# Performance work log

Hardware: AMD Instinct MI355X
Metric: run time of the kernel (lower is better)

The kernel has to match this reference:

```python
import jax, jax.numpy as jnp
import numpy as np

NEG_SLOPE = 0.2  # GATConv default leaky_relu slope


def setup_inputs() -> dict:
    key = jax.random.key(0)
    ks = jax.random.split(key, 5)
    B, C, N, H, F, k = 8, 128, 4096, 4, 128, 16
    return {
        "x": jax.random.normal(ks[0], (B, C, N, 1), dtype=jnp.float32),
        "W": jax.random.normal(ks[1], (C, H * F), dtype=jnp.float32) * 0.05,
        "att_src": jax.random.normal(ks[2], (H, F), dtype=jnp.float32) * 0.05,
        "att_dst": jax.random.normal(ks[3], (H, F), dtype=jnp.float32) * 0.05,
        "bias": jax.random.normal(ks[4], (F,), dtype=jnp.float32) * 0.05,
        "k": k,
    }


def reference(x, W, att_src, att_dst, bias, k):
    B, C, N, _ = x.shape
    H, F = att_src.shape
    xf = jnp.transpose(x[..., 0], (0, 2, 1))  # [B, N, C] node features

    # --- per-batch kNN graph in feature space (loop=True: self included) ---
    sq = jnp.sum(xf * xf, axis=-1)  # [B, N]
    # squared Euclidean distances [B, N, N]
    dist = sq[:, :, None] + sq[:, None, :] - 2.0 * jnp.einsum("bnc,bmc->bnm", xf, xf)
    _, nbr = jax.lax.top_k(-dist, k)  # [B, N, k] indices of k nearest (incl. self)

    # --- GATConv (concat=False -> average heads) ---
    h = jnp.einsum("bnc,chf->bnhf", xf, W.reshape(C, H, F))  # [B, N, H, F]
    a_src = jnp.sum(h * att_src, axis=-1)  # [B, N, H]
    a_dst = jnp.sum(h * att_dst, axis=-1)  # [B, N, H]

    gather = jax.vmap(lambda a, idx: a[idx])  # batched fancy-index
    a_src_n = gather(a_src, nbr)  # [B, N, k, H]
    h_n = gather(h, nbr)          # [B, N, k, H, F]

    e = jax.nn.leaky_relu(a_src_n + a_dst[:, :, None, :], NEG_SLOPE)  # [B, N, k, H]
    alpha = jax.nn.softmax(e, axis=2)  # softmax over each node's k incoming edges
    out = jnp.sum(alpha[..., None] * h_n, axis=2)  # [B, N, H, F]
    out = jnp.mean(out, axis=2) + bias  # [B, N, F]
    return jnp.transpose(out, (0, 2, 1))[..., None]  # [B, F, N, 1]
```

## Files before the change

### kernel.cpp

```cpp
#include <hip/hip_runtime.h>
#include <hip/hip_bf16.h>

#define BB 8
#define CC 128
#define NN 4096
#define HH 4
#define FF 128
#define KK 16
#define HF 512
#define CAPH 128
#define LCAP 32

typedef __attribute__((ext_vector_type(8))) short short8v;
typedef __attribute__((ext_vector_type(8))) unsigned short ushort8v;
typedef __attribute__((ext_vector_type(4))) float f32x4;

__device__ __forceinline__ float bf2f(unsigned int u) {
  return __uint_as_float(u << 16);
}

__device__ __forceinline__ unsigned short f2bf(float f) {
  unsigned int u = __float_as_uint(f);
  unsigned int lsb = (u >> 16) & 1u;
  u += 0x7fffu + lsb;
  return (unsigned short)(u >> 16);
}

__device__ __forceinline__ unsigned int umin2(unsigned int a, unsigned int b) {
  return a < b ? a : b;
}
__device__ __forceinline__ unsigned int umin3(unsigned int a, unsigned int b, unsigned int c) {
  return umin2(umin2(a, b), c);
}

__device__ __forceinline__ void gload16(const void* gsrc, void* ldst) {
  __builtin_amdgcn_global_load_lds(
      (const __attribute__((address_space(1))) unsigned int*)gsrc,
      (__attribute__((address_space(3))) unsigned int*)ldst, 16, 0, 0);
}

__launch_bounds__(256)
__global__ void k_split(const float* __restrict__ x,
                        float* __restrict__ xt,
                        unsigned short* __restrict__ xhi,
                        float* __restrict__ hsq) {
  __shared__ float Ls[CC][65];
  int b = blockIdx.x >> 6, nb = blockIdx.x & 63;
  int n0 = nb * 64;
  int tid = threadIdx.x;
  const float* xb = x + (size_t)b * CC * NN;

  for (int i = tid; i < CC * 64; i += 256) {
    int c = i >> 6, nl = i & 63;
    Ls[c][nl] = xb[(size_t)c * NN + n0 + nl];
  }
  __syncthreads();

  int n = tid >> 2, part = tid & 3;
  int node = b * NN + n0 + n;
  float sum = 0.f;
#pragma unroll
  for (int g = 0; g < 4; ++g) {
    float v[8];
    ushort8v ph;
#pragma unroll
    for (int j = 0; j < 8; ++j) {
      int c = part * 32 + g * 8 + j;
      v[j] = Ls[c][n];
      ph[j] = f2bf(v[j]);
      sum += v[j] * v[j];
    }
    float4 f0 = {v[0], v[1], v[2], v[3]};
    float4 f1 = {v[4], v[5], v[6], v[7]};
    *(float4*)&xt[(size_t)node * CC + part * 32 + g * 8] = f0;
    *(float4*)&xt[(size_t)node * CC + part * 32 + g * 8 + 4] = f1;
    *(ushort8v*)&xhi[(size_t)node * CC + part * 32 + g * 8] = ph;
  }
  sum += __shfl_xor(sum, 1, 64);
  sum += __shfl_xor(sum, 2, 64);
  if (part == 0) hsq[node] = 0.5f * sum;
}

__global__ void k_wpack(const float* __restrict__ W,
                        unsigned short* __restrict__ Whi,
                        unsigned short* __restrict__ Wlo) {
  int g = blockIdx.x * 256 + threadIdx.x;
  int kg = g & 3, r16 = (g >> 2) & 15, ks = (g >> 6) & 3, ct = g >> 8;
  int hf = ct * 16 + r16;
  int c0 = ks * 32 + kg * 8;
  ushort8v ph, pl;
#pragma unroll
  for (int j = 0; j < 8; ++j) {
    float v = W[(size_t)(c0 + j) * HF + hf];
    unsigned short hb = f2bf(v);
    ph[j] = hb;
    pl[j] = f2bf(v - bf2f(hb));
  }
  *(ushort8v*)&Whi[(size_t)g * 8] = ph;
  *(ushort8v*)&Wlo[(size_t)g * 8] = pl;
}

__launch_bounds__(256)
__global__ void k_tauscan(const unsigned short* __restrict__ xhi,
                          const float* __restrict__ hsq,
                          unsigned int* __restrict__ keys16) {
  __shared__ short8v AS[2][256];
  __shared__ unsigned int mv[4][16][33];
  int bx = blockIdx.x;
  int b = bx & 7, rest = bx >> 3;
  int qg = rest >> 1, sh = rest & 1;
  int w = threadIdx.x >> 6, lane = threadIdx.x & 63;
  int qcol = lane & 15, kg = lane >> 4;
  int base = b * NN;
  int q = base + qg * 64 + w * 16 + qcol;
  int t0 = sh * 32;

  const short8v* XH = (const short8v*)xhi;
  short8v bh0 = XH[(size_t)q * 16 + kg];
  short8v bh1 = XH[(size_t)q * 16 + 4 + kg];
  short8v bh2 = XH[(size_t)q * 16 + 8 + kg];
  short8v bh3 = XH[(size_t)q * 16 + 12 + kg];

  int snode = w * 4 + (lane >> 4);
  int sgran = (lane & 15) ^ (snode & 15);

  gload16(xhi + ((size_t)(base + t0 * 16 + snode)) * 128 + sgran * 8, &AS[0][w * 64]);
  __syncthreads();

  unsigned int bd[8];
  unsigned int worst = 0;
  int cur = 0;

#pragma unroll 1
  for (int lt = 0; lt < 32; ++lt) {
    if (lt + 1 < 32)
      gload16(xhi + ((size_t)(base + (t0 + lt + 1) * 16 + snode)) * 128 + sgran * 8,
              &AS[cur ^ 1][w * 64]);
    short8v ah0 = AS[cur][qcol * 16 + ((0 + kg) ^ qcol)];
    short8v ah1 = AS[cur][qcol * 16 + ((4 + kg) ^ qcol)];
    short8v ah2 = AS[cur][qcol * 16 + ((8 + kg) ^ qcol)];
    short8v ah3 = AS[cur][qcol * 16 + ((12 + kg) ^ qcol)];
    f32x4 acc = {0.f, 0.f, 0.f, 0.f};
    acc = __builtin_amdgcn_mfma_f32_16x16x32_bf16(ah0, bh0, acc, 0, 0, 0);
    acc = __builtin_amdgcn_mfma_f32_16x16x32_bf16(ah1, bh1, acc, 0, 0, 0);
    acc = __builtin_amdgcn_mfma_f32_16x16x32_bf16(ah2, bh2, acc, 0, 0, 0);
    acc = __builtin_amdgcn_mfma_f32_16x16x32_bf16(ah3, bh3, acc, 0, 0, 0);
    float4 hs = *(const float4*)&hsq[base + (t0 + lt) * 16 + kg * 4];
    float hsa[4] = {hs.x, hs.y, hs.z, hs.w};

    if (lt < 2) {
#pragma unroll
      for (int r = 0; r < 4; ++r) {
        float tv = acc[r] - hsa[r] + 512.0f;
        bd[lt * 4 + r] = (__float_as_uint(tv) & ~1023u) | (1023u - (unsigned)(lt * 4 + r));
      }
      if (lt == 1) {
        unsigned int m0 = umin3(bd[0], bd[1], bd[2]);
        m0 = umin3(m0, bd[3], bd[4]);
        m0 = umin3(m0, bd[5], bd[6]);
        worst = umin2(m0, bd[7]);
      }
    } else {
#pragma unroll
      for (int r = 0; r < 4; ++r) {
        float tv = acc[r] - hsa[r] + 512.0f;
        unsigned int key = (__float_as_uint(tv) & ~1023u) | (1023u - (unsigned)(lt * 4 + r));
        if (key > worst) {
#pragma unroll
          for (int i = 0; i < 8; ++i) bd[i] = (bd[i] == worst) ? key : bd[i];
          unsigned int m0 = umin3(bd[0], bd[1], bd[2]);
          m0 = umin3(m0, bd[3], bd[4]);
          m0 = umin3(m0, bd[5], bd[6]);
          worst = umin2(m0, bd[7]);
        }
      }
    }
    __syncthreads();
    cur ^= 1;
  }

#pragma unroll
  for (int i = 0; i < 8; ++i) mv[w][qcol][kg * 8 + i] = bd[i];
  __syncthreads();

  if (lane < 16) {
    unsigned int tb[16];
#pragma unroll
    for (int i = 0; i < 16; ++i) tb[i] = mv[w][lane][i];
    unsigned int w0 = umin3(tb[0], tb[1], tb[2]);
    w0 = umin3(w0, tb[3], tb[4]);
    w0 = umin3(w0, tb[5], tb[6]);
    w0 = umin2(w0, tb[7]);
    unsigned int w1 = umin3(tb[8], tb[9], tb[10]);
    w1 = umin3(w1, tb[11], tb[12]);
    w1 = umin3(w1, tb[13], tb[14]);
    w1 = umin2(w1, tb[15]);
    unsigned int wst = umin2(w0, w1);
    for (int j = 16; j < 32; ++j) {
      unsigned int v = mv[w][lane][j];
      if (v > wst) {
        bool done = false;
#pragma unroll
        for (int i = 0; i < 16; ++i) {
          bool m = (!done) && (tb[i] == wst);
          done = done || m;
          tb[i] = m ? v : tb[i];
        }
        unsigned int a0 = umin3(tb[0], tb[1], tb[2]);
        a0 = umin3(a0, tb[3], tb[4]);
        a0 = umin3(a0, tb[5], tb[6]);
        a0 = umin2(a0, tb[7]);
        unsigned int a1 = umin3(tb[8], tb[9], tb[10]);
        a1 = umin3(a1, tb[11], tb[12]);
        a1 = umin3(a1, tb[13], tb[14]);
        a1 = umin2(a1, tb[15]);
        wst = umin2(a0, a1);
      }
    }
    int qq = base + qg * 64 + w * 16 + lane;
    unsigned int* o = keys16 + ((size_t)qq * 2 + sh) * 16;
#pragma unroll
    for (int i = 0; i < 16; ++i) o[i] = tb[i];
  }
}

__launch_bounds__(256)
__global__ void k_taumerge(const unsigned int* __restrict__ keys16,
                           float* __restrict__ thr) {
  int q = blockIdx.x * 256 + threadIdx.x;
  const unsigned int* kp = keys16 + (size_t)q * 32;
  unsigned int tb[16];
#pragma unroll
  for (int i = 0; i < 16; ++i) tb[i] = kp[i];
  unsigned int w0 = umin3(tb[0], tb[1], tb[2]);
  w0 = umin3(w0, tb[3], tb[4]);
  w0 = umin3(w0, tb[5], tb[6]);
  w0 = umin2(w0, tb[7]);
  unsigned int w1 = umin3(tb[8], tb[9], tb[10]);
  w1 = umin3(w1, tb[11], tb[12]);
  w1 = umin3(w1, tb[13], tb[14]);
  w1 = umin2(w1, tb[15]);
  unsigned int wst = umin2(w0, w1);
#pragma unroll 1
  for (int j = 16; j < 32; ++j) {
    unsigned int v = kp[j];
    if (v > wst) {
      bool done = false;
#pragma unroll
      for (int i = 0; i < 16; ++i) {
        bool m = (!done) && (tb[i] == wst);
        done = done || m;
        tb[i] = m ? v : tb[i];
      }
      unsigned int a0 = umin3(tb[0], tb[1], tb[2]);
      a0 = umin3(a0, tb[3], tb[4]);
      a0 = umin3(a0, tb[5], tb[6]);
      a0 = umin2(a0, tb[7]);
      unsigned int a1 = umin3(tb[8], tb[9], tb[10]);
      a1 = umin3(a1, tb[11], tb[12]);
      a1 = umin3(a1, tb[13], tb[14]);
      a1 = umin2(a1, tb[15]);
      wst = umin2(a0, a1);
    }
  }
  thr[q] = __uint_as_float(wst & ~1023u) - 0.5f;
}

__launch_bounds__(256)
__global__ void k_collect2(const unsigned short* __restrict__ xhi,
                           const float* __restrict__ hsq,
                           const float* __restrict__ thr,
                           unsigned short* __restrict__ cand,
                           unsigned short* __restrict__ qcnt) {
  __shared__ short8v AS[2][2][256];
  __shared__ unsigned short lbuf[256][34];
  int bx = blockIdx.x;
  int b = bx & 7, rest = bx >> 3;
  int qg = rest >> 1, ht = rest & 1;
  int w = threadIdx.x >> 6, lane = threadIdx.x & 63;
  int tid = threadIdx.x;
  int qcol = lane & 15, kg = lane >> 4;
  int base = b * NN;
  int q = base + qg * 64 + w * 16 + qcol;

  const short8v* XH = (const short8v*)xhi;
  short8v bh0 = XH[(size_t)q * 16 + kg];
  short8v bh1 = XH[(size_t)q * 16 + 4 + kg];
  short8v bh2 = XH[(size_t)q * 16 + 8 + kg];
  short8v bh3 = XH[(size_t)q * 16 + 12 + kg];
  float myThr = thr[q];

  int snode = w * 4 + (lane >> 4);
  int sgran = (lane & 15) ^ (snode & 15);

  int tbase = ht * 128;
  gload16(xhi + ((size_t)(base + (tbase + 0) * 16 + snode)) * 128 + sgran * 8,
          &AS[0][0][w * 64]);
  gload16(xhi + ((size_t)(base + (tbase + 1) * 16 + snode)) * 128 + sgran * 8,
          &AS[0][1][w * 64]);
  __syncthreads();

  int myCnt = 0;
  int cur = 0;

#pragma unroll 1
  for (int lt = 0; lt < 128; lt += 2) {
    if (lt + 2 < 128) {
      gload16(xhi + ((size_t)(base + (tbase + lt + 2) * 16 + snode)) * 128 + sgran * 8,
              &AS[cur ^ 1][0][w * 64]);
      gload16(xhi + ((size_t)(base + (tbase + lt + 3) * 16 + snode)) * 128 + sgran * 8,
              &AS[cur ^ 1][1][w * 64]);
    }
#pragma unroll
    for (int tt = 0; tt < 2; ++tt) {
      int t = tbase + lt + tt;
      short8v ah0 = AS[cur][tt][qcol * 16 + ((0 + kg) ^ qcol)];
      short8v ah1 = AS[cur][tt][qcol * 16 + ((4 + kg) ^ qcol)];
      short8v ah2 = AS[cur][tt][qcol * 16 + ((8 + kg) ^ qcol)];
      short8v ah3 = AS[cur][tt][qcol * 16 + ((12 + kg) ^ qcol)];
      f32x4 acc = {0.f, 0.f, 0.f, 0.f};
      acc = __builtin_amdgcn_mfma_f32_16x16x32_bf16(ah0, bh0, acc, 0, 0, 0);
      acc = __builtin_amdgcn_mfma_f32_16x16x32_bf16(ah1, bh1, acc, 0, 0, 0);
      acc = __builtin_amdgcn_mfma_f32_16x16x32_bf16(ah2, bh2, acc, 0, 0, 0);
      acc = __builtin_amdgcn_mfma_f32_16x16x32_bf16(ah3, bh3, acc, 0, 0, 0);
      float4 hs = *(const float4*)&hsq[base + t * 16 + kg * 4];
      float hsa[4] = {hs.x, hs.y, hs.z, hs.w};
#pragma unroll
      for (int r = 0; r < 4; ++r) {
        float tv = acc[r] - hsa[r] + 512.0f;
        bool pass = (tv >= myThr) && (myCnt < LCAP);
        if (pass) {
          lbuf[tid][myCnt] = (unsigned short)(t * 16 + kg * 4 + r);
          ++myCnt;
        }
      }
    }
    __syncthreads();
    cur ^= 1;
  }

  int c0_ = __shfl(myCnt, qcol, 64);
  int c1_ = __shfl(myCnt, qcol + 16, 64);
  int c2_ = __shfl(myCnt, qcol + 32, 64);
  int c3_ = __shfl(myCnt, qcol + 48, 64);
  int off = (kg > 0 ? c0_ : 0) + (kg > 1 ? c1_ : 0) + (kg > 2 ? c2_ : 0);
  int tot = c0_ + c1_ + c2_ + c3_;
  unsigned short* dst = cand + (size_t)q * (2 * CAPH) + ht * CAPH + off;
#pragma unroll 1
  for (int i = 0; i < myCnt; ++i) dst[i] = lbuf[tid][i];
  if (kg == 0) qcnt[(size_t)q * 2 + ht] = (unsigned short)tot;
}

__launch_bounds__(256)
__global__ void k_rerank(const float* __restrict__ xt, const float* __restrict__ hsq,
                         const unsigned short* __restrict__ cand,
                         const unsigned short* __restrict__ qcnt,
                         unsigned short* __restrict__ nbr) {
  __shared__ unsigned long long pk[4][256];
  int w = threadIdx.x >> 6;
  int bid = blockIdx.x;
  int b = bid & 7, inner = bid >> 3;
  int wq = (b << 12) + inner * 4 + w;
  int lane = threadIdx.x & 63;
  int base = b * NN;
  int n0 = qcnt[(size_t)wq * 2];
  int n1 = qcnt[(size_t)wq * 2 + 1];
  int nt = n0 + n1;
  const float* qr = xt + (size_t)wq * CC;
  int cid = lane >> 3, part = lane & 7;

  float4 qv[4];
#pragma unroll
  for (int ph = 0; ph < 4; ++ph)
    qv[ph] = *(const float4*)&qr[ph * 32 + part * 4];

  int npass = (nt + 7) >> 3;
#pragma unroll 2
  for (int p = 0; p < npass; ++p) {
    int j = p * 8 + cid;
    bool valid = j < nt;
    int c = 0;
    if (valid)
      c = (j < n0) ? cand[(size_t)wq * (2 * CAPH) + j]
                   : cand[(size_t)wq * (2 * CAPH) + CAPH + (j - n0)];
    const float* cr = xt + (size_t)(base + c) * CC;
    float acc = 0.f;
#pragma unroll
    for (int ph = 0; ph < 4; ++ph) {
      float4 cv = *(const float4*)&cr[ph * 32 + part * 4];
      acc = fmaf(qv[ph].x, cv.x, acc);
      acc = fmaf(qv[ph].y, cv.y, acc);
      acc = fmaf(qv[ph].z, cv.z, acc);
      acc = fmaf(qv[ph].w, cv.w, acc);
    }
    acc += __shfl_xor(acc, 1, 64);
    acc += __shfl_xor(acc, 2, 64);
    acc += __shfl_xor(acc, 4, 64);
    if (part == 0) {
      float val = acc - hsq[base + c];
      unsigned int sb = __float_as_uint(val);
      sb = (sb & 0x80000000u) ? ~sb : (sb | 0x80000000u);
      unsigned long long key =
          ((unsigned long long)sb << 16) | (unsigned long long)(65535 - c);
      pk[w][p * 8 + cid] = valid ? key : 0ull;
    }
  }

  unsigned long long sk[4];
#pragma unroll
  for (int s = 0; s < 4; ++s) {
    int j = lane + s * 64;
    sk[s] = (j < nt) ? pk[w][j] : 0ull;
  }

  int rk0 = 0, rk1 = 0, rk2 = 0, rk3 = 0;
  int nslot = (nt + 63) >> 6;
  if (nslot == 1) {
#pragma unroll 4
    for (int j = 0; j < nt; ++j) {
      unsigned long long kj = pk[w][j];
      rk0 += (kj > sk[0]);
    }
  } else if (nslot == 2) {
#pragma unroll 4
    for (int j = 0; j < nt; ++j) {
      unsigned long long kj = pk[w][j];
      rk0 += (kj > sk[0]);
      rk1 += (kj > sk[1]);
    }
  } else {
#pragma unroll 2
    for (int j = 0; j < nt; ++j) {
      unsigned long long kj = pk[w][j];
      rk0 += (kj > sk[0]);
      rk1 += (kj > sk[1]);
      rk2 += (kj > sk[2]);
      rk3 += (kj > sk[3]);
    }
  }

  unsigned short* o = nbr + (size_t)wq * KK;
  {
    int j = lane;
    if (j < nt && rk0 < KK) o[rk0] = (unsigned short)(65535 - (unsigned)(sk[0] & 0xffffull));
    j = lane + 64;
    if (j < nt && rk1 < KK) o[rk1] = (unsigned short)(65535 - (unsigned)(sk[1] & 0xffffull));
    j = lane + 128;
    if (j < nt && rk2 < KK) o[rk2] = (unsigned short)(65535 - (unsigned)(sk[2] & 0xffffull));
    j = lane + 192;
    if (j < nt && rk3 < KK) o[rk3] = (unsigned short)(65535 - (unsigned)(sk[3] & 0xffffull));
  }
}

__launch_bounds__(256)
__global__ void k_h2(const float* __restrict__ xt,
                     const unsigned short* __restrict__ Whi,
                     const unsigned short* __restrict__ Wlo,
                     unsigned short* __restrict__ hout) {
  int w = threadIdx.x >> 6, lane = threadIdx.x & 63;
  int r16 = lane & 15, kg = lane >> 4;
  int nd0 = blockIdx.x * 64 + w * 16;
  const float* arow = xt + (size_t)(nd0 + r16) * CC;
  short8v ahi[4], alo[4];
#pragma unroll
  for (int ks = 0; ks < 4; ++ks) {
    float4 f0 = *(const float4*)&arow[ks * 32 + kg * 8];
    float4 f1 = *(const float4*)&arow[ks * 32 + kg * 8 + 4];
    float fv[8] = {f0.x, f0.y, f0.z, f0.w, f1.x, f1.y, f1.z, f1.w};
    short8v hh_, ll_;
#pragma unroll
    for (int j = 0; j < 8; ++j) {
      unsigned short hb = f2bf(fv[j]);
      hh_[j] = (short)hb;
      ll_[j] = (short)f2bf(fv[j] - bf2f(hb));
    }
    ahi[ks] = hh_; alo[ks] = ll_;
  }
  const short8v* WH = (const short8v*)Whi;
  const short8v* WL = (const short8v*)Wlo;
#pragma unroll 1
  for (int ct = 0; ct < 32; ++ct) {
    int hf = ct * 16 + r16;
    f32x4 acc = {0.f, 0.f, 0.f, 0.f};
#pragma unroll
    for (int ks = 0; ks < 4; ++ks) {
      size_t gidx = (size_t)(((ct * 4 + ks) * 16 + r16) * 4 + kg);
      short8v bh = WH[gidx];
      short8v bl = WL[gidx];
      acc = __builtin_amdgcn_mfma_f32_16x16x32_bf16(ahi[ks], bh, acc, 0, 0, 0);
      acc = __builtin_amdgcn_mfma_f32_16x16x32_bf16(ahi[ks], bl, acc, 0, 0, 0);
      acc = __builtin_amdgcn_mfma_f32_16x16x32_bf16(alo[ks], bh, acc, 0, 0, 0);
    }
#pragma unroll
    for (int r = 0; r < 4; ++r)
      hout[(size_t)(nd0 + kg * 4 + r) * HF + hf] = f2bf(acc[r]);
  }
}

__global__ void k_att(const unsigned short* __restrict__ h,
                      const float* __restrict__ att_src, const float* __restrict__ att_dst,
                      float* __restrict__ a_src, float* __restrict__ a_dst) {
  int gid = blockIdx.x * 256 + threadIdx.x;
  int wid = gid >> 6;
  int lane = threadIdx.x & 63;
  uint4 v = ((const uint4*)(h + (size_t)wid * HF))[lane];
  float hv[8];
  hv[0] = bf2f(v.x & 0xffff); hv[1] = bf2f(v.x >> 16);
  hv[2] = bf2f(v.y & 0xffff); hv[3] = bf2f(v.y >> 16);
  hv[4] = bf2f(v.z & 0xffff); hv[5] = bf2f(v.z >> 16);
  hv[6] = bf2f(v.w & 0xffff); hv[7] = bf2f(v.w >> 16);
  int base = lane * 8;
  float s = 0.f, d = 0.f;
#pragma unroll
  for (int i = 0; i < 8; ++i) {
    s += hv[i] * att_src[base + i];
    d += hv[i] * att_dst[base + i];
  }
#pragma unroll
  for (int off = 1; off < 16; off <<= 1) {
    s += __shfl_xor(s, off, 64);
    d += __shfl_xor(d, off, 64);
  }
  if ((lane & 15) == 0) {
    int hh = lane >> 4;
    a_src[wid * HH + hh] = s;
    a_dst[wid * HH + hh] = d;
  }
}

__launch_bounds__(256)
__global__ void k_out(const unsigned short* __restrict__ h,
                      const unsigned short* __restrict__ nbr,
                      const float* __restrict__ a_src, const float* __restrict__ a_dst,
                      const float* __restrict__ bias, float* __restrict__ out) {
  __shared__ float Ot[FF][17];
  int b = blockIdx.x & 7, nb = blockIdx.x >> 3;
  int w = threadIdx.x >> 6, lane = threadIdx.x & 63;
  int hh = lane >> 4, jj = lane & 15;

  for (int t = 0; t < 4; ++t) {
    int nl = w * 4 + t;
    int node = b * NN + nb * 16 + nl;
    int mj = nbr[node * KK + jj];

    float e = a_src[((size_t)b * NN + mj) * HH + hh] + a_dst[(size_t)node * HH + hh];
    e = e >= 0.f ? e : 0.2f * e;
    float m = e;
#pragma unroll
    for (int off = 1; off < 16; off <<= 1) m = fmaxf(m, __shfl_xor(m, off, 64));
    float p = expf(e - m);
    float sum = p;
#pragma unroll
    for (int off = 1; off < 16; off <<= 1) sum += __shfl_xor(sum, off, 64);
    float alpha = p / sum;

    float acc[8];
#pragma unroll
    for (int i = 0; i < 8; ++i) acc[i] = 0.f;

#pragma unroll
    for (int j = 0; j < 16; ++j) {
      float aj = __shfl(alpha, (hh << 4) | j, 64);
      int m2 = __shfl(mj, j, 64);
      uint4 v = ((const uint4*)(h + (size_t)(b * NN + m2) * HF))[lane];
      acc[0] += aj * bf2f(v.x & 0xffff); acc[1] += aj * bf2f(v.x >> 16);
      acc[2] += aj * bf2f(v.y & 0xffff); acc[3] += aj * bf2f(v.y >> 16);
      acc[4] += aj * bf2f(v.z & 0xffff); acc[5] += aj * bf2f(v.z >> 16);
      acc[6] += aj * bf2f(v.w & 0xffff); acc[7] += aj * bf2f(v.w >> 16);
    }

#pragma unroll
    for (int i = 0; i < 8; ++i) {
      acc[i] += __shfl_xor(acc[i], 16, 64);
      acc[i] += __shfl_xor(acc[i], 32, 64);
    }
    if (hh == 0) {
#pragma unroll
      for (int i = 0; i < 8; ++i) Ot[jj * 8 + i][nl] = acc[i] * 0.25f;
    }
  }
  __syncthreads();

#pragma unroll
  for (int it = 0; it < 8; ++it) {
    int idx = it * 256 + threadIdx.x;
    int f = idx >> 4, nl = idx & 15;
    out[((size_t)b * FF + f) * NN + nb * 16 + nl] = Ot[f][nl] + bias[f];
  }
}

extern "C" void kernel_launch(void* const* d_in, const int* in_sizes, int n_in,
                              void* d_out, int out_size, void* d_ws, size_t ws_size,
                              hipStream_t stream) {
  const float* x       = (const float*)d_in[0];
  const float* W       = (const float*)d_in[1];
  const float* att_src = (const float*)d_in[2];
  const float* att_dst = (const float*)d_in[3];
  const float* bias    = (const float*)d_in[4];

  char* ws = (char*)d_ws;
  float* xt            = (float*)ws;
  unsigned short* xhi  = (unsigned short*)(ws + 16777216);
  unsigned int* keys16 = (unsigned int*)(ws + 25165824);
  unsigned short* cand = (unsigned short*)(ws + 25165824);
  unsigned short* h    = (unsigned short*)(ws + 16777216);
  unsigned short* nbr  = (unsigned short*)(ws + 50331648);
  unsigned short* qcnt = (unsigned short*)(ws + 51380224);
  float* thr   = (float*)(ws + 51511296);
  float* hsq   = (float*)(ws + 51642368);
  float* a_src = (float*)(ws + 51773440);
  unsigned short* Whi  = (unsigned short*)(ws + 51773440);
  unsigned short* Wlo  = (unsigned short*)(ws + 51773440 + 131072);
  float* a_dst = (float*)(ws + 52297728);

  float* out = (float*)d_out;

  k_split   <<<BB * (NN / 64), 256, 0, stream>>>(x, xt, xhi, hsq);
  k_wpack   <<<HF * CC / 8 / 256, 256, 0, stream>>>(W, Whi, Wlo);
  k_tauscan <<<BB * 64 * 2, 256, 0, stream>>>(xhi, hsq, keys16);
  k_taumerge<<<BB * NN / 256, 256, 0, stream>>>(keys16, thr);
  k_collect2<<<BB * 64 * 2, 256, 0, stream>>>(xhi, hsq, thr, cand, qcnt);
  k_rerank  <<<BB * NN / 4, 256, 0, stream>>>(xt, hsq, cand, qcnt, nbr);
  k_h2      <<<BB * NN / 64, 256, 0, stream>>>(xt, Whi, Wlo, h);
  k_att     <<<BB * NN / 4, 256, 0, stream>>>(h, att_src, att_dst, a_src, a_dst);
  k_out     <<<BB * (NN / 16), 256, 0, stream>>>(h, nbr, a_src, a_dst, bias, out);
}
```

Measured before the change: 292.5 us.

## Reuse each LDS A-tile across two query groups per wave in candidate collection

The candidate-collection kernel now gives each wave two 16-query column groups, so each A fragment read from LDS feeds two sets of MFMAs. Waves are split by tile parity: each wave pair handles alternate tiles and stages its own half of the tile. This halves LDS fragment reads and loop iterations per MFMA. The trade-off is a smaller per-list capacity (22 instead of 32 entries per thread per query), a cross-wave prefix sum over shared counts, and clamping at CAPH, which changes overflow behaviour.

```diff
diff --git a/kernel.cpp b/kernel.cpp
--- a/kernel.cpp
+++ b/kernel.cpp
@@ -9,7 +9,7 @@
 #define KK 16
 #define HF 512
 #define CAPH 128
-#define LCAP 32
+#define LCAP2 22
 
 typedef __attribute__((ext_vector_type(8))) short short8v;
 typedef __attribute__((ext_vector_type(8))) unsigned short ushort8v;
@@ -273,82 +273,121 @@
                            unsigned short* __restrict__ cand,
                            unsigned short* __restrict__ qcnt) {
   __shared__ short8v AS[2][2][256];
-  __shared__ unsigned short lbuf[256][34];
+  __shared__ unsigned short lbuf[256][2][22];
+  __shared__ unsigned short cnts[256][2];
   int bx = blockIdx.x;
   int b = bx & 7, rest = bx >> 3;
   int qg = rest >> 1, ht = rest & 1;
   int w = threadIdx.x >> 6, lane = threadIdx.x & 63;
   int tid = threadIdx.x;
+  int u = w & 1, p = w >> 1;
   int qcol = lane & 15, kg = lane >> 4;
   int base = b * NN;
-  int q = base + qg * 64 + w * 16 + qcol;
+  int q0 = base + qg * 64 + u * 32 + qcol;
+  int q1 = q0 + 16;
 
   const short8v* XH = (const short8v*)xhi;
-  short8v bh0 = XH[(size_t)q * 16 + kg];
-  short8v bh1 = XH[(size_t)q * 16 + 4 + kg];
-  short8v bh2 = XH[(size_t)q * 16 + 8 + kg];
-  short8v bh3 = XH[(size_t)q * 16 + 12 + kg];
-  float myThr = thr[q];
-
-  int snode = w * 4 + (lane >> 4);
-  int sgran = (lane & 15) ^ (snode & 15);
+  short8v bh0 = XH[(size_t)q0 * 16 + kg];
+  short8v bh1 = XH[(size_t)q0 * 16 + 4 + kg];
+  short8v bh2 = XH[(size_t)q0 * 16 + 8 + kg];
+  short8v bh3 = XH[(size_t)q0 * 16 + 12 + kg];
+  short8v ch0 = XH[(size_t)q1 * 16 + kg];
+  short8v ch1 = XH[(size_t)q1 * 16 + 4 + kg];
+  short8v ch2 = XH[(size_t)q1 * 16 + 8 + kg];
+  short8v ch3 = XH[(size_t)q1 * 16 + 12 + kg];
+  float thr0 = thr[q0], thr1 = thr[q1];
+
+  int s0 = u * 128 + lane;
+  int s1 = u * 128 + 64 + lane;
+  int nd0_ = s0 >> 4, gr0_ = (s0 & 15) ^ (nd0_ & 15);
+  int nd1_ = s1 >> 4, gr1_ = (s1 & 15) ^ (nd1_ & 15);
 
   int tbase = ht * 128;
-  gload16(xhi + ((size_t)(base + (tbase + 0) * 16 + snode)) * 128 + sgran * 8,
-          &AS[0][0][w * 64]);
-  gload16(xhi + ((size_t)(base + (tbase + 1) * 16 + snode)) * 128 + sgran * 8,
-          &AS[0][1][w * 64]);
+  {
+    int t = tbase + p;
+    gload16(xhi + ((size_t)(base + t * 16 + nd0_)) * 128 + gr0_ * 8,
+            &AS[p][0][u * 128]);
+    gload16(xhi + ((size_t)(base + t * 16 + nd1_)) * 128 + gr1_ * 8,
+            &AS[p][0][u * 128 + 64]);
+  }
   __syncthreads();
 
-  int myCnt = 0;
+  int cnt0 = 0, cnt1 = 0;
   int cur = 0;
 
 #pragma unroll 1
-  for (int lt = 0; lt < 128; lt += 2) {
-    if (lt + 2 < 128) {
-      gload16(xhi + ((size_t)(base + (tbase + lt + 2) * 16 + snode)) * 128 + sgran * 8,
-              &AS[cur ^ 1][0][w * 64]);
-      gload16(xhi + ((size_t)(base + (tbase + lt + 3) * 16 + snode)) * 128 + sgran * 8,
-              &AS[cur ^ 1][1][w * 64]);
-    }
-#pragma unroll
-    for (int tt = 0; tt < 2; ++tt) {
-      int t = tbase + lt + tt;
-      short8v ah0 = AS[cur][tt][qcol * 16 + ((0 + kg) ^ qcol)];
-      short8v ah1 = AS[cur][tt][qcol * 16 + ((4 + kg) ^ qcol)];
-      short8v ah2 = AS[cur][tt][qcol * 16 + ((8 + kg) ^ qcol)];
-      short8v ah3 = AS[cur][tt][qcol * 16 + ((12 + kg) ^ qcol)];
-      f32x4 acc = {0.f, 0.f, 0.f, 0.f};
-      acc = __builtin_amdgcn_mfma_f32_16x16x32_bf16(ah0, bh0, acc, 0, 0, 0);
-      acc = __builtin_amdgcn_mfma_f32_16x16x32_bf16(ah1, bh1, acc, 0, 0, 0);
-      acc = __builtin_amdgcn_mfma_f32_16x16x32_bf16(ah2, bh2, acc, 0, 0, 0);
-      acc = __builtin_amdgcn_mfma_f32_16x16x32_bf16(ah3, bh3, acc, 0, 0, 0);
-      float4 hs = *(const float4*)&hsq[base + t * 16 + kg * 4];
-      float hsa[4] = {hs.x, hs.y, hs.z, hs.w};
-#pragma unroll
-      for (int r = 0; r < 4; ++r) {
-        float tv = acc[r] - hsa[r] + 512.0f;
-        bool pass = (tv >= myThr) && (myCnt < LCAP);
-        if (pass) {
-          lbuf[tid][myCnt] = (unsigned short)(t * 16 + kg * 4 + r);
-          ++myCnt;
-        }
+  for (int it = 0; it < 64; ++it) {
+    int t = tbase + it * 2 + p;
+    if (it + 1 < 64) {
+      int tn = t + 2;
+      gload16(xhi + ((size_t)(base + tn * 16 + nd0_)) * 128 + gr0_ * 8,
+              &AS[p][cur ^ 1][u * 128]);
+      gload16(xhi + ((size_t)(base + tn * 16 + nd1_)) * 128 + gr1_ * 8,
+              &AS[p][cur ^ 1][u * 128 + 64]);
+    }
+    short8v ah0 = AS[p][cur][qcol * 16 + ((0 + kg) ^ qcol)];
+    short8v ah1 = AS[p][cur][qcol * 16 + ((4 + kg) ^ qcol)];
+    short8v ah2 = AS[p][cur][qcol * 16 + ((8 + kg) ^ qcol)];
+    short8v ah3 = AS[p][cur][qcol * 16 + ((12 + kg) ^ qcol)];
+    f32x4 a0 = {0.f, 0.f, 0.f, 0.f};
+    a0 = __builtin_amdgcn_mfma_f32_16x16x32_bf16(ah0, bh0, a0, 0, 0, 0);
+    a0 = __builtin_amdgcn_mfma_f32_16x16x32_bf16(ah1, bh1, a0, 0, 0, 0);
+    a0 = __builtin_amdgcn_mfma_f32_16x16x32_bf16(ah2, bh2, a0, 0, 0, 0);
+    a0 = __builtin_amdgcn_mfma_f32_16x16x32_bf16(ah3, bh3, a0, 0, 0, 0);
+    f32x4 a1 = {0.f, 0.f, 0.f, 0.f};
+    a1 = __builtin_amdgcn_mfma_f32_16x16x32_bf16(ah0, ch0, a1, 0, 0, 0);
+    a1 = __builtin_amdgcn_mfma_f32_16x16x32_bf16(ah1, ch1, a1, 0, 0, 0);
+    a1 = __builtin_amdgcn_mfma_f32_16x16x32_bf16(ah2, ch2, a1, 0, 0, 0);
+    a1 = __builtin_amdgcn_mfma_f32_16x16x32_bf16(ah3, ch3, a1, 0, 0, 0);
+    float4 hs = *(const float4*)&hsq[base + t * 16 + kg * 4];
+    float hsa[4] = {hs.x, hs.y, hs.z, hs.w};
+#pragma unroll
+    for (int r = 0; r < 4; ++r) {
+      unsigned short ci = (unsigned short)(t * 16 + kg * 4 + r);
+      float tv0 = a0[r] - hsa[r] + 512.0f;
+      if (tv0 >= thr0 && cnt0 < LCAP2) {
+        lbuf[tid][0][cnt0] = ci;
+        ++cnt0;
+      }
+      float tv1 = a1[r] - hsa[r] + 512.0f;
+      if (tv1 >= thr1 && cnt1 < LCAP2) {
+        lbuf[tid][1][cnt1] = ci;
+        ++cnt1;
       }
     }
     __syncthreads();
     cur ^= 1;
   }
 
-  int c0_ = __shfl(myCnt, qcol, 64);
-  int c1_ = __shfl(myCnt, qcol + 16, 64);
-  int c2_ = __shfl(myCnt, qcol + 32, 64);
-  int c3_ = __shfl(myCnt, qcol + 48, 64);
-  int off = (kg > 0 ? c0_ : 0) + (kg > 1 ? c1_ : 0) + (kg > 2 ? c2_ : 0);
-  int tot = c0_ + c1_ + c2_ + c3_;
-  unsigned short* dst = cand + (size_t)q * (2 * CAPH) + ht * CAPH + off;
+  cnts[tid][0] = (unsigned short)cnt0;
+  cnts[tid][1] = (unsigned short)cnt1;
+  __syncthreads();
+
+  int myo = p * 4 + kg;
+#pragma unroll
+  for (int s = 0; s < 2; ++s) {
+    int q = base + qg * 64 + u * 32 + s * 16 + qcol;
+    int off = 0, tot = 0;
+#pragma unroll
+    for (int o2 = 0; o2 < 8; ++o2) {
+      int p2 = o2 >> 2, kg2 = o2 & 3;
+      int ctid = (p2 * 2 + u) * 64 + kg2 * 16 + qcol;
+      int c = (int)cnts[ctid][s];
+      if (o2 < myo) off += c;
+      tot += c;
+    }
+    int myCnt = (s == 0) ? cnt0 : cnt1;
+    unsigned short* dst = cand + (size_t)q * (2 * CAPH) + ht * CAPH;
 #pragma unroll 1
-  for (int i = 0; i < myCnt; ++i) dst[i] = lbuf[tid][i];
-  if (kg == 0) qcnt[(size_t)q * 2 + ht] = (unsigned short)tot;
+    for (int i = 0; i < myCnt; ++i) {
+      int pos = off + i;
+      if (pos < CAPH) dst[pos] = lbuf[tid][s][i];
+    }
+    if (myo == 0) {
+      if (tot > CAPH) tot = CAPH;
+      qcnt[(size_t)q * 2 + ht] = (unsigned short)tot;
+    }
+  }
 }
 
 __launch_bounds__(256)
```

New measurement: 289.3 us. About the same (-1.1%).
